# Performance work log

Hardware: AMD Instinct MI355X
Metric: run time of the kernel (lower is better)

Reference implementation:

```python
import jax, jax.numpy as jnp
import numpy as np

B, LQ, LK, D, H = 4, 2048, 2048, 1024, 16
HD = D // H  # head dim = 64


def setup_inputs() -> dict:
    key = jax.random.key(0)
    ks = jax.random.split(key, 8)
    s = 1.0 / np.sqrt(D)
    return {
        "zt": jax.random.normal(ks[0], (B, LQ, D), jnp.float32),
        "ic": jax.random.normal(ks[1], (B, LK, D), jnp.float32),
        "Wq": jax.random.normal(ks[2], (D, D), jnp.float32) * s,
        "bq": jax.random.normal(ks[3], (D,), jnp.float32) * 0.01,
        "Wk": jax.random.normal(ks[4], (D, D), jnp.float32) * s,
        "bk": jax.random.normal(ks[5], (D,), jnp.float32) * 0.01,
        "Wv": jax.random.normal(ks[6], (D, D), jnp.float32) * s,
        "bv": jax.random.normal(ks[7], (D,), jnp.float32) * 0.01,
    }


def reference(zt, ic, Wq, bq, Wk, bk, Wv, bv):
    # Linear projections (torch Linear: x @ W.T + b); weights here stored as [out, in]
    q = zt @ Wq.T + bq            # [B, LQ, D]
    k = ic @ Wk.T + bk            # [B, LK, D]
    v = ic @ Wv.T + bv            # [B, LK, D]
    # split heads -> [B, H, L, HD]
    q = q.reshape(B, LQ, H, HD).transpose(0, 2, 1, 3)
    k = k.reshape(B, LK, H, HD).transpose(0, 2, 1, 3)
    v = v.reshape(B, LK, H, HD).transpose(0, 2, 1, 3)
    scale = 1.0 / jnp.sqrt(jnp.asarray(HD, q.dtype))
    scores = jnp.einsum('bhqd,bhkd->bhqk', q, k) * scale  # [B, H, LQ, LK]
    attn = jax.nn.softmax(scores, axis=-1)
    out = jnp.einsum('bhqk,bhkd->bhqd', attn, v)          # [B, H, LQ, HD]
    return out.transpose(0, 2, 1, 3).reshape(B, LQ, D)
```

## Files before the change

### kernel.cpp

```cpp
#include <hip/hip_runtime.h>
#include <hip/hip_bf16.h>
#include <cstdint>

#define B_  4
#define LQ_ 2048
#define LK_ 2048
#define D_  1024
#define H_  16
#define HD_ 64

typedef __attribute__((ext_vector_type(8))) short bf16x8;
typedef __attribute__((ext_vector_type(4))) float f32x4;

#if defined(__has_builtin)
#if __has_builtin(__builtin_amdgcn_exp2f)
#define EXP2F(x) __builtin_amdgcn_exp2f(x)
#else
#define EXP2F(x) exp2f(x)
#endif
#else
#define EXP2F(x) exp2f(x)
#endif

__device__ __forceinline__ unsigned short f2b(float f) {
    union { float f; unsigned u; } v; v.f = f;
    unsigned u = v.u;
    unsigned r = (u + 0x7fffu + ((u >> 16) & 1u)) >> 16;
    return (unsigned short)r;
}

__device__ __forceinline__ void gl_lds16(const unsigned short* g, unsigned short* l) {
    __builtin_amdgcn_global_load_lds(
        (const __attribute__((address_space(1))) unsigned int*)(g),
        (__attribute__((address_space(3))) unsigned int*)(l),
        16, 0, 0);
}

__global__ void cvt_all(const float* __restrict__ a0, unsigned short* __restrict__ d0,
                        const float* __restrict__ a1, unsigned short* __restrict__ d1,
                        const float* __restrict__ w0, unsigned short* __restrict__ e0, float s0,
                        const float* __restrict__ w1, unsigned short* __restrict__ e1,
                        const float* __restrict__ w2, unsigned short* __restrict__ e2,
                        int nact, int nw) {
    const float* in; unsigned short* out; float s = 1.0f; int n;
    switch (blockIdx.y) {
        case 0: in = a0; out = d0; n = nact; break;
        case 1: in = a1; out = d1; n = nact; break;
        case 2: in = w0; out = e0; n = nw; s = s0; break;
        case 3: in = w1; out = e1; n = nw; break;
        default: in = w2; out = e2; n = nw; break;
    }
    int i = (blockIdx.x * blockDim.x + threadIdx.x) * 8;
    int stride = gridDim.x * blockDim.x * 8;
    for (; i < n; i += stride) {
        float4 x = *(const float4*)(in + i);
        float4 y = *(const float4*)(in + i + 4);
        bf16x8 v;
        v[0] = (short)f2b(x.x * s); v[1] = (short)f2b(x.y * s);
        v[2] = (short)f2b(x.z * s); v[3] = (short)f2b(x.w * s);
        v[4] = (short)f2b(y.x * s); v[5] = (short)f2b(y.y * s);
        v[6] = (short)f2b(y.z * s); v[7] = (short)f2b(y.w * s);
        *(bf16x8*)(out + i) = v;
    }
}

__global__ __launch_bounds__(256) void qkv_gemm(
    const unsigned short* __restrict__ Xq,
    const unsigned short* __restrict__ Xkv,
    const unsigned short* __restrict__ Wqb, const unsigned short* __restrict__ Wkb,
    const unsigned short* __restrict__ Wvb,
    const float* __restrict__ bq, const float* __restrict__ bk,
    const float* __restrict__ bv, float qscale,
    unsigned short* __restrict__ Qb, unsigned short* __restrict__ Kb,
    unsigned short* __restrict__ Vb)
{
    __shared__ unsigned short As[16 * 512];
    __shared__ unsigned short Bs[16 * 512];

    const int proj = blockIdx.x >> 3;
    const int nt0  = blockIdx.x & 7;
    const unsigned short* X = (proj == 0) ? Xq : Xkv;
    const unsigned short* W = (proj == 0) ? Wqb : (proj == 1 ? Wkb : Wvb);
    const float* bias       = (proj == 0) ? bq  : (proj == 1 ? bk  : bv);
    unsigned short* Y       = (proj == 0) ? Qb  : (proj == 1 ? Kb  : Vb);
    const float bscale      = (proj == 0) ? qscale : 1.0f;

    const int tid  = threadIdx.x;
    const int lane = tid & 63;
    const int w    = tid >> 6;
    const int wm   = w & 1, wn = w >> 1;
    const int m0   = blockIdx.y * 128;
    const int n0   = nt0 * 128;
    const int l15  = lane & 15, quad = lane >> 4;

    f32x4 acc[4][4] = {};

    const unsigned short* gA[4];
    const unsigned short* gB[4];
    unsigned short* lA[4];
    unsigned short* lB[4];
    #pragma unroll
    for (int j = 0; j < 4; ++j) {
        int rt = w + (j >> 1) * 4, kblk = j & 1;
        int f = rt * 2 + kblk;
        gA[j] = X + (size_t)(m0 + rt * 16 + l15) * 1024 + kblk * 32 + quad * 8;
        gB[j] = W + (size_t)(n0 + rt * 16 + l15) * 1024 + kblk * 32 + quad * 8;
        lA[j] = &As[f * 512 + lane * 8];
        lB[j] = &Bs[f * 512 + lane * 8];
    }
    const unsigned short* frA = &As[(wm * 4) * 1024 + lane * 8];
    const unsigned short* frB = &Bs[(wn * 4) * 1024 + lane * 8];

    for (int k0 = 0; k0 < 1024; k0 += 64) {
        __syncthreads();
        #pragma unroll
        for (int j = 0; j < 4; ++j) {
            gl_lds16(gA[j] + k0, lA[j]);
            gl_lds16(gB[j] + k0, lB[j]);
        }
        __syncthreads();

        #pragma unroll
        for (int kblk = 0; kblk < 2; ++kblk) {
            bf16x8 af[4], bf[4];
            #pragma unroll
            for (int mt = 0; mt < 4; ++mt)
                af[mt] = *(const bf16x8*)(frA + mt * 1024 + kblk * 512);
            #pragma unroll
            for (int nt = 0; nt < 4; ++nt)
                bf[nt] = *(const bf16x8*)(frB + nt * 1024 + kblk * 512);
            #pragma unroll
            for (int mt = 0; mt < 4; ++mt)
                #pragma unroll
                for (int nt = 0; nt < 4; ++nt)
                    acc[mt][nt] = __builtin_amdgcn_mfma_f32_16x16x32_bf16(
                        af[mt], bf[nt], acc[mt][nt], 0, 0, 0);
        }
    }

    float bvv[4];
    #pragma unroll
    for (int nt = 0; nt < 4; ++nt)
        bvv[nt] = bias[n0 + wn * 64 + nt * 16 + l15] * bscale;

    #pragma unroll
    for (int mt = 0; mt < 4; ++mt) {
        #pragma unroll
        for (int r = 0; r < 4; ++r) {
            int row = m0 + wm * 64 + mt * 16 + quad * 4 + r;
            unsigned short* yp = Y + (size_t)row * 1024 + n0 + wn * 64;
            #pragma unroll
            for (int nt = 0; nt < 4; ++nt)
                yp[nt * 16 + l15] = f2b(acc[mt][nt][r] + bvv[nt]);
        }
    }
}

__global__ __launch_bounds__(256) void transpose_v(
    const unsigned short* __restrict__ Vb, unsigned short* __restrict__ Vt)
{
    __shared__ unsigned short L[64 * 72];
    const int t0 = blockIdx.x * 64, h = blockIdx.y, b = blockIdx.z;
    const int rr = threadIdx.x >> 3;
    const int cc = (threadIdx.x & 7) * 8;

    #pragma unroll
    for (int p = 0; p < 2; ++p) {
        int r = rr + p * 32;
        *(bf16x8*)(&L[r * 72 + cc]) =
            *(const bf16x8*)(Vb + (size_t)(b * 2048 + t0 + r) * 1024 + h * 64 + cc);
    }
    __syncthreads();
    #pragma unroll
    for (int p = 0; p < 2; ++p) {
        int d = rr + p * 32;
        bf16x8 v;
        #pragma unroll
        for (int j = 0; j < 8; ++j)
            v[j] = (short)L[(cc + j) * 72 + d];
        *(bf16x8*)(Vt + ((size_t)(b * 16 + h) * 64 + d) * 2048 + t0 + cc) = v;
    }
}

__global__ __launch_bounds__(256, 2) void attn_kernel(
    const unsigned short* __restrict__ Q,
    const unsigned short* __restrict__ Kp,
    const unsigned short* __restrict__ Vt,
    float* __restrict__ Out)
{
    __shared__ unsigned short Ks[16 * 512];
    __shared__ unsigned short Vs[16 * 512];
    __shared__ unsigned short Ps[4][4096];

    const int tid  = threadIdx.x;
    const int lane = tid & 63;
    const int w    = tid >> 6;
    const int l15  = lane & 15, quad = lane >> 4;
    const int b = blockIdx.z, h = blockIdx.y, qt = blockIdx.x;

    bf16x8 qf[4][2];
    #pragma unroll
    for (int half = 0; half < 4; ++half) {
        const unsigned short* qptr =
            Q + (size_t)(b * LQ_ + qt * 256 + w * 64 + half * 16 + l15) * 1024 + h * 64;
        qf[half][0] = *(const bf16x8*)(qptr + quad * 8);
        qf[half][1] = *(const bf16x8*)(qptr + 32 + quad * 8);
    }

    bf16x8 ones;
    #pragma unroll
    for (int j = 0; j < 8; ++j) ones[j] = (short)0x3F80;

    f32x4 oacc[4][4] = {};
    f32x4 lacc[4]    = {};

    const unsigned short* Kbase = Kp + (size_t)b * LK_ * 1024 + h * 64;
    const unsigned short* Vbase = Vt + (size_t)(b * 16 + h) * 64 * 2048;

    const unsigned short* gK[4];
    unsigned short* lK[4];
    const unsigned short* gV[4];
    unsigned short* lV[4];
    #pragma unroll
    for (int j = 0; j < 4; ++j) {
        int kt = w + (j >> 1) * 4, dblk = j & 1;
        gK[j] = Kbase + (size_t)(kt * 16 + l15) * 1024 + dblk * 32 + quad * 8;
        lK[j] = &Ks[(kt * 2 + dblk) * 512 + lane * 8];
        gV[j] = Vbase + (size_t)(w * 16 + l15) * 2048 + j * 32 + quad * 8;
        lV[j] = &Vs[(w * 4 + j) * 512 + lane * 8];
    }

    const int pws = (quad >> 1) * 128 + l15 * 8 + (quad & 1) * 4;
    unsigned short* PwB = &Ps[w][pws];
    const unsigned short* PrB = &Ps[w][lane * 8];
    const unsigned short* Kfr = &Ks[lane * 8];
    const unsigned short* Vfr = &Vs[lane * 8];

    for (int k0 = 0; k0 < LK_; k0 += 128) {
        __syncthreads();
        #pragma unroll
        for (int j = 0; j < 4; ++j) {
            gl_lds16(gK[j] + (size_t)k0 * 1024, lK[j]);
            gl_lds16(gV[j] + k0, lV[j]);
        }
        __syncthreads();

        #pragma unroll
        for (int cc = 0; cc < 2; ++cc) {
            f32x4 st[4][4] = {};
            #pragma unroll
            for (int t = 0; t < 4; ++t)
                #pragma unroll
                for (int dblk = 0; dblk < 2; ++dblk) {
                    bf16x8 kf = *(const bf16x8*)(Kfr + ((cc * 4 + t) * 2 + dblk) * 512);
                    #pragma unroll
                    for (int half = 0; half < 4; ++half)
                        st[half][t] = __builtin_amdgcn_mfma_f32_16x16x32_bf16(
                            kf, qf[half][dblk], st[half][t], 0, 0, 0);
                }

            #pragma unroll
            for (int half = 0; half < 4; ++half) {
                unsigned short* pw = PwB + half * 1024;
                #pragma unroll
                for (int t = 0; t < 4; ++t) {
                    unsigned u0 = __float_as_uint(EXP2F(st[half][t][0])) + 0x8000u;
                    unsigned u1 = __float_as_uint(EXP2F(st[half][t][1])) + 0x8000u;
                    unsigned u2 = __float_as_uint(EXP2F(st[half][t][2])) + 0x8000u;
                    unsigned u3 = __float_as_uint(EXP2F(st[half][t][3])) + 0x8000u;
                    uint2 pk;
                    pk.x = __builtin_amdgcn_perm(u1, u0, 0x07060302);
                    pk.y = __builtin_amdgcn_perm(u3, u2, 0x07060302);
                    *(uint2*)(pw + t * 256) = pk;
                }
            }

            #pragma unroll
            for (int hbl = 0; hbl < 2; ++hbl) {
                bf16x8 pf[4];
                #pragma unroll
                for (int half = 0; half < 4; ++half) {
                    pf[half] = *(const bf16x8*)(PrB + half * 1024 + hbl * 512);
                    lacc[half] = __builtin_amdgcn_mfma_f32_16x16x32_bf16(
                        pf[half], ones, lacc[half], 0, 0, 0);
                }
                int hb = cc * 2 + hbl;
                #pragma unroll
                for (int nt = 0; nt < 4; ++nt) {
                    bf16x8 vf = *(const bf16x8*)(Vfr + (nt * 4 + hb) * 512);
                    #pragma unroll
                    for (int half = 0; half < 4; ++half)
                        oacc[half][nt] = __builtin_amdgcn_mfma_f32_16x16x32_bf16(
                            pf[half], vf, oacc[half][nt], 0, 0, 0);
                }
            }
        }
    }

    #pragma unroll
    for (int half = 0; half < 4; ++half) {
        float il[4];
        #pragma unroll
        for (int r = 0; r < 4; ++r) il[r] = 1.0f / lacc[half][r];
        #pragma unroll
        for (int nt = 0; nt < 4; ++nt) {
            #pragma unroll
            for (int r = 0; r < 4; ++r) {
                size_t orow = (size_t)(b * LQ_ + qt * 256 + w * 64 + half * 16 + quad * 4 + r);
                Out[orow * 1024 + h * 64 + nt * 16 + l15] = oacc[half][nt][r] * il[r];
            }
        }
    }
}

extern "C" void kernel_launch(void* const* d_in, const int* in_sizes, int n_in,
                              void* d_out, int out_size, void* d_ws, size_t ws_size,
                              hipStream_t stream) {
    const float* zt = (const float*)d_in[0];
    const float* ic = (const float*)d_in[1];
    const float* Wq = (const float*)d_in[2];
    const float* bq = (const float*)d_in[3];
    const float* Wk = (const float*)d_in[4];
    const float* bk = (const float*)d_in[5];
    const float* Wv = (const float*)d_in[6];
    const float* bv = (const float*)d_in[7];
    float* out = (float*)d_out;

    const size_t M8 = (size_t)8192 * 1024;
    const size_t M1 = (size_t)1024 * 1024;
    unsigned short* Qb  = (unsigned short*)d_ws;
    unsigned short* Kb  = Qb  + M8;
    unsigned short* Vb  = Kb  + M8;
    unsigned short* Xz  = Vb  + M8;
    unsigned short* Xi  = Xz  + M8;
    unsigned short* Wqb = Xi  + M8;
    unsigned short* Wkb = Wqb + M1;
    unsigned short* Wvb = Wkb + M1;
    unsigned short* Vtb = Xz;

    const float qscale = 0.125f * 1.44269504088896f;

    dim3 gcv(4096, 5);
    cvt_all<<<gcv, 256, 0, stream>>>(zt, Xz, ic, Xi,
                                     Wq, Wqb, qscale, Wk, Wkb, Wv, Wvb,
                                     (int)M8, (int)M1);

    dim3 gproj(24, 64);
    qkv_gemm<<<gproj, 256, 0, stream>>>(Xz, Xi, Wqb, Wkb, Wvb,
                                        bq, bk, bv, qscale, Qb, Kb, Vb);

    dim3 gtr(32, 16, 4);
    transpose_v<<<gtr, 256, 0, stream>>>(Vb, Vtb);

    dim3 gattn(8, 16, 4);
    attn_kernel<<<gattn, 256, 0, stream>>>(Qb, Kb, Vtb, out);
}
```

Baseline: 317.9 us.

## Rewrite QKV GEMM as 256x256 tile with 4-slot LDS prefetch pipeline

The QKV projection GEMM moves from 128x128 tiles with 256 threads and a load-then-compute loop to 256x256 tiles with 512 threads. It uses a four-slot LDS ring, filled asynchronously three stages ahead, with explicit vmcnt waits, scheduling barriers and setprio around the MFMA phases. This is meant to hide global-to-LDS latency behind matrix math and raise reuse per loaded tile. The cost is 128KB of LDS per block and only 384 blocks, which risks occupancy and wave-quantisation losses.

```diff
diff --git a/kernel.cpp b/kernel.cpp
--- a/kernel.cpp
+++ b/kernel.cpp
@@ -35,6 +35,15 @@
         (__attribute__((address_space(3))) unsigned int*)(l),
         16, 0, 0);
 }
+
+#define PHASE_BARRIER() do { \
+    __builtin_amdgcn_sched_barrier(0); \
+    __builtin_amdgcn_s_barrier(); \
+    __builtin_amdgcn_sched_barrier(0); } while (0)
+
+#define WAITVM(N) do { \
+    asm volatile("s_waitcnt vmcnt(" #N ")" ::: "memory"); \
+    __builtin_amdgcn_sched_barrier(0); } while (0)
 
 __global__ void cvt_all(const float* __restrict__ a0, unsigned short* __restrict__ d0,
                         const float* __restrict__ a1, unsigned short* __restrict__ d1,
@@ -64,7 +73,7 @@
     }
 }
 
-__global__ __launch_bounds__(256) void qkv_gemm(
+__global__ __launch_bounds__(512, 2) void qkv_gemm(
     const unsigned short* __restrict__ Xq,
     const unsigned short* __restrict__ Xkv,
     const unsigned short* __restrict__ Wqb, const unsigned short* __restrict__ Wkb,
@@ -74,11 +83,11 @@
     unsigned short* __restrict__ Qb, unsigned short* __restrict__ Kb,
     unsigned short* __restrict__ Vb)
 {
-    __shared__ unsigned short As[16 * 512];
-    __shared__ unsigned short Bs[16 * 512];
-
-    const int proj = blockIdx.x >> 3;
-    const int nt0  = blockIdx.x & 7;
+    __shared__ unsigned short AS[4][8192];
+    __shared__ unsigned short BS[4][8192];
+
+    const int proj = blockIdx.y >> 2;
+    const int nt0  = blockIdx.y & 3;
     const unsigned short* X = (proj == 0) ? Xq : Xkv;
     const unsigned short* W = (proj == 0) ? Wqb : (proj == 1 ? Wkb : Wvb);
     const float* bias       = (proj == 0) ? bq  : (proj == 1 ? bk  : bv);
@@ -89,69 +98,116 @@
     const int lane = tid & 63;
     const int w    = tid >> 6;
     const int wm   = w & 1, wn = w >> 1;
-    const int m0   = blockIdx.y * 128;
-    const int n0   = nt0 * 128;
+    const int m0   = blockIdx.x * 256;
+    const int n0   = nt0 * 256;
     const int l15  = lane & 15, quad = lane >> 4;
 
-    f32x4 acc[4][4] = {};
-
-    const unsigned short* gA[4];
-    const unsigned short* gB[4];
-    unsigned short* lA[4];
-    unsigned short* lB[4];
-    #pragma unroll
-    for (int j = 0; j < 4; ++j) {
-        int rt = w + (j >> 1) * 4, kblk = j & 1;
-        int f = rt * 2 + kblk;
-        gA[j] = X + (size_t)(m0 + rt * 16 + l15) * 1024 + kblk * 32 + quad * 8;
-        gB[j] = W + (size_t)(n0 + rt * 16 + l15) * 1024 + kblk * 32 + quad * 8;
-        lA[j] = &As[f * 512 + lane * 8];
-        lB[j] = &Bs[f * 512 + lane * 8];
-    }
-    const unsigned short* frA = &As[(wm * 4) * 1024 + lane * 8];
-    const unsigned short* frB = &Bs[(wn * 4) * 1024 + lane * 8];
-
-    for (int k0 = 0; k0 < 1024; k0 += 64) {
-        __syncthreads();
-        #pragma unroll
-        for (int j = 0; j < 4; ++j) {
-            gl_lds16(gA[j] + k0, lA[j]);
-            gl_lds16(gB[j] + k0, lB[j]);
-        }
-        __syncthreads();
-
-        #pragma unroll
-        for (int kblk = 0; kblk < 2; ++kblk) {
-            bf16x8 af[4], bf[4];
-            #pragma unroll
-            for (int mt = 0; mt < 4; ++mt)
-                af[mt] = *(const bf16x8*)(frA + mt * 1024 + kblk * 512);
-            #pragma unroll
-            for (int nt = 0; nt < 4; ++nt)
-                bf[nt] = *(const bf16x8*)(frB + nt * 1024 + kblk * 512);
-            #pragma unroll
-            for (int mt = 0; mt < 4; ++mt)
-                #pragma unroll
-                for (int nt = 0; nt < 4; ++nt)
-                    acc[mt][nt] = __builtin_amdgcn_mfma_f32_16x16x32_bf16(
-                        af[mt], bf[nt], acc[mt][nt], 0, 0, 0);
-        }
-    }
+    f32x4 acc[8][4] = {};
+
+    const unsigned short* gA0 = X + (size_t)(m0 + (w * 2) * 16 + l15) * 1024 + quad * 8;
+    const unsigned short* gA1 = gA0 + 16 * 1024;
+    const unsigned short* gB0 = W + (size_t)(n0 + (w * 2) * 16 + l15) * 1024 + quad * 8;
+    const unsigned short* gB1 = gB0 + 16 * 1024;
+
+#define STAGE_A(slot, koff) do { \
+    gl_lds16(gA0 + (koff), &AS[slot][(w * 2) * 512 + lane * 8]); \
+    gl_lds16(gA1 + (koff), &AS[slot][(w * 2 + 1) * 512 + lane * 8]); } while (0)
+#define STAGE_B(slot, koff) do { \
+    gl_lds16(gB0 + (koff), &BS[slot][(w * 2) * 512 + lane * 8]); \
+    gl_lds16(gB1 + (koff), &BS[slot][(w * 2 + 1) * 512 + lane * 8]); } while (0)
+
+    const int aoff = (wm * 8) * 512 + lane * 8;
+    const int boff = (wn * 4) * 512 + lane * 8;
+
+    STAGE_A(0, 0);   STAGE_B(0, 0);
+    STAGE_A(1, 32);  STAGE_B(1, 32);
+    STAGE_A(2, 64);  STAGE_B(2, 64);
+    WAITVM(8);
+    __builtin_amdgcn_s_barrier();
+    __builtin_amdgcn_sched_barrier(0);
+
+    #pragma unroll 2
+    for (int t = 0; t < 16; ++t) {
+        const int s0 = (2 * t) & 3;
+        const int s1 = (2 * t + 1) & 3;
+        const int s3 = (2 * t + 3) & 3;
+
+        bf16x8 af[8], bf0, bf1;
+
+        #pragma unroll
+        for (int i = 0; i < 8; ++i)
+            af[i] = *(const bf16x8*)(&AS[s0][aoff + i * 512]);
+        bf0 = *(const bf16x8*)(&BS[s0][boff]);
+        bf1 = *(const bf16x8*)(&BS[s0][boff + 512]);
+        PHASE_BARRIER();
+        __builtin_amdgcn_s_setprio(1);
+        #pragma unroll
+        for (int i = 0; i < 8; ++i) {
+            acc[i][0] = __builtin_amdgcn_mfma_f32_16x16x32_bf16(af[i], bf0, acc[i][0], 0, 0, 0);
+            acc[i][1] = __builtin_amdgcn_mfma_f32_16x16x32_bf16(af[i], bf1, acc[i][1], 0, 0, 0);
+        }
+        __builtin_amdgcn_s_setprio(0);
+        if (t < 15) STAGE_A(s3, (t + 1) * 64 + 32);
+
+        bf0 = *(const bf16x8*)(&BS[s0][boff + 1024]);
+        bf1 = *(const bf16x8*)(&BS[s0][boff + 1536]);
+        if (t < 14) { WAITVM(6); } else { WAITVM(0); }
+        PHASE_BARRIER();
+        __builtin_amdgcn_s_setprio(1);
+        #pragma unroll
+        for (int i = 0; i < 8; ++i) {
+            acc[i][2] = __builtin_amdgcn_mfma_f32_16x16x32_bf16(af[i], bf0, acc[i][2], 0, 0, 0);
+            acc[i][3] = __builtin_amdgcn_mfma_f32_16x16x32_bf16(af[i], bf1, acc[i][3], 0, 0, 0);
+        }
+        __builtin_amdgcn_s_setprio(0);
+        if (t < 15) STAGE_B(s3, (t + 1) * 64 + 32);
+
+        #pragma unroll
+        for (int i = 0; i < 8; ++i)
+            af[i] = *(const bf16x8*)(&AS[s1][aoff + i * 512]);
+        bf0 = *(const bf16x8*)(&BS[s1][boff]);
+        bf1 = *(const bf16x8*)(&BS[s1][boff + 512]);
+        PHASE_BARRIER();
+        __builtin_amdgcn_s_setprio(1);
+        #pragma unroll
+        for (int i = 0; i < 8; ++i) {
+            acc[i][0] = __builtin_amdgcn_mfma_f32_16x16x32_bf16(af[i], bf0, acc[i][0], 0, 0, 0);
+            acc[i][1] = __builtin_amdgcn_mfma_f32_16x16x32_bf16(af[i], bf1, acc[i][1], 0, 0, 0);
+        }
+        __builtin_amdgcn_s_setprio(0);
+        if (t < 14) STAGE_A(s0, (t + 2) * 64);
+
+        bf0 = *(const bf16x8*)(&BS[s1][boff + 1024]);
+        bf1 = *(const bf16x8*)(&BS[s1][boff + 1536]);
+        if (t < 14) { WAITVM(6); } else if (t == 14) { WAITVM(4); }
+        PHASE_BARRIER();
+        __builtin_amdgcn_s_setprio(1);
+        #pragma unroll
+        for (int i = 0; i < 8; ++i) {
+            acc[i][2] = __builtin_amdgcn_mfma_f32_16x16x32_bf16(af[i], bf0, acc[i][2], 0, 0, 0);
+            acc[i][3] = __builtin_amdgcn_mfma_f32_16x16x32_bf16(af[i], bf1, acc[i][3], 0, 0, 0);
+        }
+        __builtin_amdgcn_s_setprio(0);
+        if (t < 14) STAGE_B(s0, (t + 2) * 64);
+    }
+
+#undef STAGE_A
+#undef STAGE_B
 
     float bvv[4];
     #pragma unroll
-    for (int nt = 0; nt < 4; ++nt)
-        bvv[nt] = bias[n0 + wn * 64 + nt * 16 + l15] * bscale;
-
-    #pragma unroll
-    for (int mt = 0; mt < 4; ++mt) {
+    for (int j = 0; j < 4; ++j)
+        bvv[j] = bias[n0 + wn * 64 + j * 16 + l15] * bscale;
+
+    #pragma unroll
+    for (int i = 0; i < 8; ++i) {
         #pragma unroll
         for (int r = 0; r < 4; ++r) {
-            int row = m0 + wm * 64 + mt * 16 + quad * 4 + r;
+            int row = m0 + wm * 128 + i * 16 + quad * 4 + r;
             unsigned short* yp = Y + (size_t)row * 1024 + n0 + wn * 64;
             #pragma unroll
-            for (int nt = 0; nt < 4; ++nt)
-                yp[nt * 16 + l15] = f2b(acc[mt][nt][r] + bvv[nt]);
+            for (int j = 0; j < 4; ++j)
+                yp[j * 16 + l15] = f2b(acc[i][j][r] + bvv[j]);
         }
     }
 }
@@ -345,8 +401,8 @@
                                      Wq, Wqb, qscale, Wk, Wkb, Wv, Wvb,
                                      (int)M8, (int)M1);
 
-    dim3 gproj(24, 64);
-    qkv_gemm<<<gproj, 256, 0, stream>>>(Xz, Xi, Wqb, Wkb, Wvb,
+    dim3 gproj(32, 12);
+    qkv_gemm<<<gproj, 512, 0, stream>>>(Xz, Xi, Wqb, Wkb, Wvb,
                                         bq, bk, bv, qscale, Qb, Kb, Vb);
 
     dim3 gtr(32, 16, 4);
```

New measurement: 304.4 us. 1.04x faster.
